# Performance work log

Hardware: AMD Instinct MI355X
Metric: run time of the kernel (lower is better)

Reference implementation:

```python
import jax, jax.numpy as jnp
import numpy as np
from jax import lax

VOCAB = 32000
EMB = 64
HID = 512
B, T = 8, 512


def _glorot(key, shape):
    fan_in, fan_out = shape[0], shape[-1]
    s = jnp.sqrt(2.0 / (fan_in + fan_out)).astype(jnp.float32)
    return jax.random.normal(key, shape, dtype=jnp.float32) * s


def setup_inputs() -> dict:
    key = jax.random.key(0)
    ks = jax.random.split(key, 8)
    inputs = jax.random.randint(ks[0], (B, T), 0, VOCAB)
    emb = jax.random.normal(ks[1], (VOCAB, EMB), dtype=jnp.float32) * 0.02
    W1 = _glorot(ks[2], (EMB, 3 * HID))
    b1 = jnp.zeros((3 * HID,), dtype=jnp.float32)
    W2 = _glorot(ks[3], (HID, 3 * HID))
    b2 = jnp.zeros((3 * HID,), dtype=jnp.float32)
    Wp = _glorot(ks[4], (HID, VOCAB))
    bp = jnp.zeros((VOCAB,), dtype=jnp.float32)
    return {"inputs": inputs, "emb": emb, "W1": W1, "b1": b1,
            "W2": W2, "b2": b2, "Wp": Wp, "bp": bp}


def qrnn_layer(x, W, b):
    # x: [T, B, D] -> h: [T, B, H]; QRNN fo-pool
    g = jnp.einsum('tbd,dh->tbh', x, W) + b  # [T, B, 3H]
    z, f, o = jnp.split(g, 3, axis=-1)
    z = jnp.tanh(z)
    f = jax.nn.sigmoid(f)
    o = jax.nn.sigmoid(o)

    def step(c, zf):
        z_t, f_t = zf
        c = f_t * c + (1.0 - f_t) * z_t
        return c, c

    c0 = jnp.zeros_like(z[0])
    _, cs = lax.scan(step, c0, (z, f))  # cs: [T, B, H]
    return o * cs


def reference(inputs, emb, W1, b1, W2, b2, Wp, bp):
    x = emb[inputs]                  # [B, T, E]
    x = jnp.transpose(x, (1, 0, 2))  # [T, B, E]
    x = qrnn_layer(x, W1, b1)        # [T, B, H]
    x = qrnn_layer(x, W2, b2)        # [T, B, H]
    x = jnp.transpose(x, (1, 0, 2))  # [B, T, H]
    logits = jnp.einsum('bth,hv->btv', x, Wp) + bp  # [B, T, V]
    return logits
```

## Files before the change

kernel.cpp:

```cpp
#include <hip/hip_runtime.h>
#include <math.h>

#define BB 8
#define TT 512
#define EE 64
#define HH 512
#define VV 32000
#define MM 4096
#define G3 1536

typedef _Float16 half8 __attribute__((ext_vector_type(8)));
typedef float floatx4 __attribute__((ext_vector_type(4)));

__device__ __forceinline__ void gld_lds16(const _Float16* g, _Float16* l) {
    __builtin_amdgcn_global_load_lds(
        (const __attribute__((address_space(1))) void*)(const void*)g,
        (__attribute__((address_space(3))) void*)(void*)l, 16, 0, 0);
}

__global__ __launch_bounds__(256) void transpose_f32_f16(
    const float* __restrict__ W, _Float16* __restrict__ Wt, int K, int N)
{
    __shared__ float tile[32][33];
    const int n0 = blockIdx.x * 32;
    const int k0 = blockIdx.y * 32;
    const int tx = threadIdx.x, ty = threadIdx.y;
    #pragma unroll
    for (int i = 0; i < 32; i += 8)
        tile[ty + i][tx] = W[(k0 + ty + i) * N + n0 + tx];
    __syncthreads();
    #pragma unroll
    for (int i = 0; i < 32; i += 8)
        Wt[(n0 + ty + i) * K + k0 + tx] = (_Float16)tile[tx][ty + i];
}

__global__ __launch_bounds__(256) void gather_embed(
    const int* __restrict__ ids, const float* __restrict__ emb,
    _Float16* __restrict__ x)
{
    const int tid = blockIdx.x * 256 + threadIdx.x;
    const int m = tid >> 6, e = tid & 63;
    const int t = m >> 3, b = m & 7;
    const int id = ids[b * TT + t];
    x[tid] = (_Float16)emb[id * EE + e];
}

__global__ __launch_bounds__(256) void gemm_f16(
    const _Float16* __restrict__ A, const _Float16* __restrict__ Bt,
    const float* __restrict__ bias, float* __restrict__ C,
    int Ndim, int Kdim, int act)
{
    __shared__ _Float16 As[128 * 64];
    __shared__ _Float16 Bs[128 * 64];

    const int nb  = gridDim.x, mbl = gridDim.y;
    const int bid = blockIdx.y * nb + blockIdx.x;
    const int sw  = (bid & 7) * ((nb * mbl) >> 3) + (bid >> 3);
    const int n0 = (sw / mbl) * 128;
    const int m0 = (sw % mbl) * 128;
    const int tid = threadIdx.x;
    const int wid = tid >> 6;
    const int lane = tid & 63;
    const int wm = wid & 1, wn = wid >> 1;
    const int quad = lane >> 4, rlo = lane & 15;

    floatx4 acc[4][4] = {};

    for (int k0 = 0; k0 < Kdim; k0 += 64) {
        __syncthreads();
        #pragma unroll
        for (int i = 0; i < 4; ++i) {
            const int sbase = wid * 256 + i * 64;
            const int slot = sbase + lane;
            const int r = slot >> 3;
            const int p = slot & 7;
            const int srcg = p ^ (r & 7);
            gld_lds16(A  + (m0 + r) * Kdim + k0 + srcg * 8, As + sbase * 8);
            gld_lds16(Bt + (n0 + r) * Kdim + k0 + srcg * 8, Bs + sbase * 8);
        }
        __syncthreads();

        #pragma unroll
        for (int kk = 0; kk < 64; kk += 32) {
            const int gi = (kk >> 3) + quad;
            half8 af[4], bf[4];
            #pragma unroll
            for (int mi = 0; mi < 4; ++mi) {
                const int ra = wm * 64 + mi * 16 + rlo;
                af[mi] = *(const half8*)(As + (ra * 8 + (gi ^ (ra & 7))) * 8);
            }
            #pragma unroll
            for (int ni = 0; ni < 4; ++ni) {
                const int rb = wn * 64 + ni * 16 + rlo;
                bf[ni] = *(const half8*)(Bs + (rb * 8 + (gi ^ (rb & 7))) * 8);
            }
            #pragma unroll
            for (int mi = 0; mi < 4; ++mi)
                #pragma unroll
                for (int ni = 0; ni < 4; ++ni)
                    acc[mi][ni] = __builtin_amdgcn_mfma_f32_16x16x32_f16(
                        af[mi], bf[ni], acc[mi][ni], 0, 0, 0);
        }
    }

    #pragma unroll
    for (int ni = 0; ni < 4; ++ni) {
        const int gn = n0 + wn * 64 + ni * 16 + rlo;
        const float bv = bias[gn];
        #pragma unroll
        for (int mi = 0; mi < 4; ++mi) {
            const int gm = m0 + wm * 64 + mi * 16 + quad * 4;
            #pragma unroll
            for (int r = 0; r < 4; ++r) {
                float v = acc[mi][ni][r] + bv;
                if (act)
                    v = (gn < HH) ? tanhf(v) : 1.f / (1.f + expf(-v));
                C[(gm + r) * Ndim + gn] = v;
            }
        }
    }
}

#define NCHUNK 16
#define CHPB 16
#define CHL (TT / NCHUNK)

__global__ __launch_bounds__(256) void fo_pool_scan(
    const float* __restrict__ g, _Float16* __restrict__ hout,
    int base_mult, int t_stride)
{
    __shared__ float sA[NCHUNK][CHPB];
    __shared__ float sB[NCHUNK][CHPB];
    const int c_idx = threadIdx.x & (CHPB - 1);
    const int chunk = threadIdx.x >> 4;
    const int ch = blockIdx.x * CHPB + c_idx;
    const int b = ch >> 9, h = ch & 511;
    const int t0 = chunk * CHL;
    const float* gp = g + (size_t)(t0 * BB + b) * G3 + h;

    float c = 0.f, Aa = 1.f;
    {
        const float* p = gp;
        #pragma unroll 8
        for (int t = 0; t < CHL; ++t) {
            const float z = p[0];
            const float f = p[HH];
            c = f * c + (1.f - f) * z;
            Aa *= f;
            p += BB * G3;
        }
    }
    sA[chunk][c_idx] = Aa;
    sB[chunk][c_idx] = c;
    __syncthreads();

    float carry = 0.f;
    #pragma unroll
    for (int j = 0; j < NCHUNK - 1; ++j)
        if (j < chunk) carry = sA[j][c_idx] * carry + sB[j][c_idx];

    c = carry;
    int oidx = b * base_mult + h + t0 * t_stride;
    const float* p = gp;
    #pragma unroll 8
    for (int t = 0; t < CHL; ++t) {
        const float z = p[0];
        const float f = p[HH];
        const float o = p[2 * HH];
        c = f * c + (1.f - f) * z;
        hout[oidx] = (_Float16)(o * c);
        p += BB * G3;
        oidx += t_stride;
    }
}

extern "C" void kernel_launch(void* const* d_in, const int* in_sizes, int n_in,
                              void* d_out, int out_size, void* d_ws, size_t ws_size,
                              hipStream_t stream) {
    (void)in_sizes; (void)n_in; (void)out_size; (void)ws_size;
    const int*   ids = (const int*)d_in[0];
    const float* emb = (const float*)d_in[1];
    const float* W1  = (const float*)d_in[2];
    const float* b1  = (const float*)d_in[3];
    const float* W2  = (const float*)d_in[4];
    const float* b2  = (const float*)d_in[5];
    const float* Wp  = (const float*)d_in[6];
    const float* bp  = (const float*)d_in[7];
    float* out = (float*)d_out;

    char* ws = (char*)d_ws;
    _Float16* x_h  = (_Float16*)(ws);
    _Float16* W1t  = (_Float16*)(ws + 524288);
    _Float16* W2t  = (_Float16*)(ws + 720896);
    _Float16* Wpt  = (_Float16*)(ws + 2293760);
    float*    gbuf = (float*)   (ws + 35061760);
    _Float16* h1   = (_Float16*)(ws + 60227584);
    _Float16* h2   = (_Float16*)(ws + 64421888);

    transpose_f32_f16<<<dim3(G3 / 32, EE / 32), dim3(32, 8), 0, stream>>>(W1, W1t, EE, G3);
    transpose_f32_f16<<<dim3(G3 / 32, HH / 32), dim3(32, 8), 0, stream>>>(W2, W2t, HH, G3);
    transpose_f32_f16<<<dim3(VV / 32, HH / 32), dim3(32, 8), 0, stream>>>(Wp, Wpt, HH, VV);
    gather_embed<<<MM * EE / 256, 256, 0, stream>>>(ids, emb, x_h);

    gemm_f16<<<dim3(G3 / 128, MM / 128), 256, 0, stream>>>(x_h, W1t, b1, gbuf, G3, EE, 1);
    fo_pool_scan<<<MM / CHPB, 256, 0, stream>>>(gbuf, h1, HH, BB * HH);
    gemm_f16<<<dim3(G3 / 128, MM / 128), 256, 0, stream>>>(h1, W2t, b2, gbuf, G3, HH, 1);
    fo_pool_scan<<<MM / CHPB, 256, 0, stream>>>(gbuf, h2, TT * HH, HH);
    gemm_f16<<<dim3(VV / 128, MM / 128), 256, 0, stream>>>(h2, Wpt, bp, out, VV, HH, 0);
}
```

Baseline: 888.7 us.

## Double-buffer GEMM LDS tiles with K=32 steps and nontemporal logits stores

The GEMM now keeps two LDS buffers and issues global-to-LDS loads for the next K=32 slice while MFMAs run on the current one, replacing the load-barrier-compute pattern that serialized memory and math. The LDS swizzle is reworked so two 32-wide rows pack into one 64-element line. The final logits GEMM writes its output with nontemporal stores to limit cache pollution from the large output. Risks: smaller K steps mean more barriers per tile, and the waitcnt/barrier placement via inline asm must correctly order LDS reads against the next overwrite.

```diff
diff --git a/kernel.cpp b/kernel.cpp
--- a/kernel.cpp
+++ b/kernel.cpp
@@ -50,8 +50,8 @@
     const float* __restrict__ bias, float* __restrict__ C,
     int Ndim, int Kdim, int act)
 {
-    __shared__ _Float16 As[128 * 64];
-    __shared__ _Float16 Bs[128 * 64];
+    __shared__ __align__(16) _Float16 As[2][4096];
+    __shared__ __align__(16) _Float16 Bs[2][4096];
 
     const int nb  = gridDim.x, mbl = gridDim.y;
     const int bid = blockIdx.y * nb + blockIdx.x;
@@ -64,43 +64,65 @@
     const int wm = wid & 1, wn = wid >> 1;
     const int quad = lane >> 4, rlo = lane & 15;
 
+    const _Float16* asrc[2];
+    const _Float16* bsrc[2];
+    int dstg[2];
+    #pragma unroll
+    for (int i = 0; i < 2; ++i) {
+        const int slot = i * 256 + wid * 64 + lane;
+        const int pr = slot >> 3, sp = slot & 7;
+        const int s  = sp ^ (pr & 7);
+        const int r  = pr * 2 + (s >> 2);
+        const int g  = s & 3;
+        asrc[i] = A  + (size_t)(m0 + r) * Kdim + g * 8;
+        bsrc[i] = Bt + (size_t)(n0 + r) * Kdim + g * 8;
+        dstg[i] = (i * 256 + wid * 64) * 8;
+    }
+
     floatx4 acc[4][4] = {};
-
-    for (int k0 = 0; k0 < Kdim; k0 += 64) {
-        __syncthreads();
-        #pragma unroll
-        for (int i = 0; i < 4; ++i) {
-            const int sbase = wid * 256 + i * 64;
-            const int slot = sbase + lane;
-            const int r = slot >> 3;
-            const int p = slot & 7;
-            const int srcg = p ^ (r & 7);
-            gld_lds16(A  + (m0 + r) * Kdim + k0 + srcg * 8, As + sbase * 8);
-            gld_lds16(Bt + (n0 + r) * Kdim + k0 + srcg * 8, Bs + sbase * 8);
-        }
-        __syncthreads();
-
-        #pragma unroll
-        for (int kk = 0; kk < 64; kk += 32) {
-            const int gi = (kk >> 3) + quad;
-            half8 af[4], bf[4];
+    const int NT = Kdim >> 5;
+
+    #pragma unroll
+    for (int i = 0; i < 2; ++i) {
+        gld_lds16(asrc[i], &As[0][dstg[i]]);
+        gld_lds16(bsrc[i], &Bs[0][dstg[i]]);
+    }
+    asm volatile("s_waitcnt vmcnt(0)\n\ts_barrier" ::: "memory");
+
+    for (int t = 0; t < NT; ++t) {
+        const int cur = t & 1;
+        if (t + 1 < NT) {
+            const int k1 = (t + 1) << 5;
             #pragma unroll
-            for (int mi = 0; mi < 4; ++mi) {
-                const int ra = wm * 64 + mi * 16 + rlo;
-                af[mi] = *(const half8*)(As + (ra * 8 + (gi ^ (ra & 7))) * 8);
+            for (int i = 0; i < 2; ++i) {
+                gld_lds16(asrc[i] + k1, &As[cur ^ 1][dstg[i]]);
+                gld_lds16(bsrc[i] + k1, &Bs[cur ^ 1][dstg[i]]);
             }
+        }
+
+        half8 af[4], bf[4];
+        #pragma unroll
+        for (int mi = 0; mi < 4; ++mi) {
+            const int ra = wm * 64 + mi * 16 + rlo;
+            const int pr = ra >> 1;
+            const int sp = (((ra & 1) << 2) | quad) ^ (pr & 7);
+            af[mi] = *(const half8*)(&As[cur][(pr * 8 + sp) * 8]);
+        }
+        #pragma unroll
+        for (int ni = 0; ni < 4; ++ni) {
+            const int rb = wn * 64 + ni * 16 + rlo;
+            const int pr = rb >> 1;
+            const int sp = (((rb & 1) << 2) | quad) ^ (pr & 7);
+            bf[ni] = *(const half8*)(&Bs[cur][(pr * 8 + sp) * 8]);
+        }
+        #pragma unroll
+        for (int mi = 0; mi < 4; ++mi)
             #pragma unroll
-            for (int ni = 0; ni < 4; ++ni) {
-                const int rb = wn * 64 + ni * 16 + rlo;
-                bf[ni] = *(const half8*)(Bs + (rb * 8 + (gi ^ (rb & 7))) * 8);
-            }
-            #pragma unroll
-            for (int mi = 0; mi < 4; ++mi)
-                #pragma unroll
-                for (int ni = 0; ni < 4; ++ni)
-                    acc[mi][ni] = __builtin_amdgcn_mfma_f32_16x16x32_f16(
-                        af[mi], bf[ni], acc[mi][ni], 0, 0, 0);
-        }
+            for (int ni = 0; ni < 4; ++ni)
+                acc[mi][ni] = __builtin_amdgcn_mfma_f32_16x16x32_f16(
+                    af[mi], bf[ni], acc[mi][ni], 0, 0, 0);
+
+        asm volatile("s_waitcnt vmcnt(0)\n\ts_barrier" ::: "memory");
     }
 
     #pragma unroll
@@ -113,9 +135,12 @@
             #pragma unroll
             for (int r = 0; r < 4; ++r) {
                 float v = acc[mi][ni][r] + bv;
-                if (act)
+                if (act) {
                     v = (gn < HH) ? tanhf(v) : 1.f / (1.f + expf(-v));
-                C[(gm + r) * Ndim + gn] = v;
+                    C[(size_t)(gm + r) * Ndim + gn] = v;
+                } else {
+                    __builtin_nontemporal_store(v, &C[(size_t)(gm + r) * Ndim + gn]);
+                }
             }
         }
     }
```

Result: no change. 875.1 us (-1.5%).
